# Optimization experiments

Hardware: AMD Instinct MI355X
Metric: run time of the kernel (lower is better)

## Reference

```python
import jax, jax.numpy as jnp
import numpy as np

B, T, D, H, W = 4096, 101, 64, 64, 32

# Tsit5 Butcher tableau (Tsitouras 2011), as used by diffrax.Tsit5
A21 = 0.161
A31, A32 = -0.008480655492356989, 0.335480655492357
A41, A42, A43 = 2.8971530571054935, -6.359448489975075, 4.3622954328695815
A51, A52, A53, A54 = 5.325864828439257, -11.748883564062828, 7.4955393428898365, -0.09249506636175525
A61, A62, A63, A64, A65 = 5.86145544294642, -12.92096931784711, 8.159367898576159, -0.071584973281401, -0.028269050394068383
# 5th-order solution weights (b7 = 0)
B1, B2, B3, B4, B5, B6 = 0.09646076681806523, 0.01, 0.4798896504144996, 1.379008574103742, -3.290069515436081, 2.324710524099774


def _mlp(y, W1, b1, W2, b2, W3, b3):
    # eqx.nn.MLP(hidden, hidden, width=32, depth=2, tanh): two tanh hidden layers
    h = jnp.tanh(y @ W1.T + b1)
    h = jnp.tanh(h @ W2.T + b2)
    return h @ W3.T + b3


def _tsit5_step(z, dt, p):
    f = lambda y: _mlp(y, *p)  # autonomous vector field (ignores t)
    k1 = f(z)
    k2 = f(z + dt * (A21 * k1))
    k3 = f(z + dt * (A31 * k1 + A32 * k2))
    k4 = f(z + dt * (A41 * k1 + A42 * k2 + A43 * k3))
    k5 = f(z + dt * (A51 * k1 + A52 * k2 + A53 * k3 + A54 * k4))
    k6 = f(z + dt * (A61 * k1 + A62 * k2 + A63 * k3 + A64 * k4 + A65 * k5))
    return z + dt * (B1 * k1 + B2 * k2 + B3 * k3 + B4 * k4 + B5 * k5 + B6 * k6)


def setup_inputs() -> dict:
    key = jax.random.key(0)
    ks = jax.random.split(key, 9)
    s = lambda fan_in: 1.0 / np.sqrt(fan_in)
    return {
        "ts": jnp.arange(T, dtype=jnp.float32) * 0.1,  # grid aligned with dt0=0.1
        "y0_batch": jax.random.normal(ks[0], (B, D), dtype=jnp.float32),
        "enc_W": jax.random.normal(ks[1], (H, D), dtype=jnp.float32) * s(D),
        "enc_b": jax.random.normal(ks[2], (H,), dtype=jnp.float32) * s(D),
        "W1": jax.random.normal(ks[3], (W, H), dtype=jnp.float32) * s(H),
        "b1": jnp.zeros((W,), dtype=jnp.float32),
        "W2": jax.random.normal(ks[4], (W, W), dtype=jnp.float32) * s(W),
        "b2": jnp.zeros((W,), dtype=jnp.float32),
        "W3": jax.random.normal(ks[5], (H, W), dtype=jnp.float32) * s(W),
        "b3": jnp.zeros((H,), dtype=jnp.float32),
        "dec_W": jax.random.normal(ks[6], (D, H), dtype=jnp.float32) * s(H),
        "dec_b": jax.random.normal(ks[7], (D,), dtype=jnp.float32) * s(H),
    }


def reference(ts, y0_batch, enc_W, enc_b, W1, b1, W2, b2, W3, b3, dec_W, dec_b):
    z0 = y0_batch @ enc_W.T + enc_b  # [B, H]
    n_steps = ts.shape[0] - 1
    dt = (ts[-1] - ts[0]) / n_steps  # == 0.1, matches dt0 with ConstantStepSize
    p = (W1, b1, W2, b2, W3, b3)

    def step(z, _):
        z1 = _tsit5_step(z, dt, p)
        return z1, z1

    _, zs_rest = jax.lax.scan(step, z0, None, length=n_steps)  # [T-1, B, H]
    zs = jnp.concatenate([z0[None], zs_rest], axis=0)  # [T, B, H]
    zs = jnp.swapaxes(zs, 0, 1)  # [B, T, H]
    ys = zs @ dec_W.T + dec_b  # [B, T, D]
    return ys, zs
```

## Files before the change

### kernel.cpp

```cpp
#include <hip/hip_runtime.h>


typedef __attribute__((ext_vector_type(8))) _Float16 half8;
typedef __attribute__((ext_vector_type(4))) float f32x4;

static constexpr int TN = 101;
static constexpr int BN = 4096;

#define MFMA(a, b, c) __builtin_amdgcn_mfma_f32_16x16x32_f16((a), (b), (c), 0, 0, 0)

__device__ __forceinline__ float tanh_pre(float x) {
  float e = __builtin_amdgcn_exp2f(x);
  float r = __builtin_amdgcn_rcpf(e + 1.0f);
  return __builtin_fmaf(-2.0f, r, 1.0f);
}

__device__ __forceinline__ void split8(const float* v, half8& hi, half8& lo) {
#pragma unroll
  for (int j = 0; j < 8; ++j) {
    _Float16 h = (_Float16)v[j];
    hi[j] = h;
    lo[j] = (_Float16)(v[j] - (float)h);
  }
}

__device__ __forceinline__ void load_wfrag(const float* __restrict__ W, int C, int row, int q,
                                           int kt, float scale, half8& hi, half8& lo) {
  const float* p = W + row * C + kt * 32 + 4 * q;
  float v[8] __attribute__((aligned(16)));
  *(f32x4*)(v) = *(const f32x4*)(p);
  *(f32x4*)(v + 4) = *(const f32x4*)(p + 16);
#pragma unroll
  for (int j = 0; j < 8; ++j) v[j] *= scale;
  split8(v, hi, lo);
}

__global__ __launch_bounds__(64, 1) void node_kernel(
    const float* __restrict__ ts, const float* __restrict__ y0,
    const float* __restrict__ encW, const float* __restrict__ encb,
    const float* __restrict__ W1, const float* __restrict__ b1,
    const float* __restrict__ W2, const float* __restrict__ b2,
    const float* __restrict__ W3, const float* __restrict__ b3,
    const float* __restrict__ decW, const float* __restrict__ decb,
    float* __restrict__ out) {
  const int l = threadIdx.x;
  const int lm = l & 15;
  const int q = l >> 4;
  const int eg = blockIdx.x * 16 + lm;

  const float TS = 2.8853900817779268f;

  const float dt = (ts[TN - 1] - ts[0]) / (float)(TN - 1);
  const float c21 = dt * 0.161f;
  const float c31 = dt * -0.008480655492356989f, c32 = dt * 0.335480655492357f;
  const float c41 = dt * 2.8971530571054935f, c42 = dt * -6.359448489975075f,
              c43 = dt * 4.3622954328695815f;
  const float c51 = dt * 5.325864828439257f, c52 = dt * -11.748883564062828f,
              c53 = dt * 7.4955393428898365f, c54 = dt * -0.09249506636175525f;
  const float c61 = dt * 5.86145544294642f, c62 = dt * -12.92096931784711f,
              c63 = dt * 8.159367898576159f, c64 = dt * -0.071584973281401f,
              c65 = dt * -0.028269050394068383f;
  const float d1 = dt * 0.09646076681806523f, d2 = dt * 0.01f, d3 = dt * 0.4798896504144996f,
              d4 = dt * 1.379008574103742f, d5 = dt * -3.290069515436081f,
              d6 = dt * 2.324710524099774f;
  const float sg3 = dt * 0.327f, sg4 = dt * 0.9f, sg5 = dt * 0.9800255409045097f,
              sg6 = dt * 1.0f;

  half8 w2h[2], w2l[2], w3h[4], w3l[4];
#pragma unroll
  for (int mt = 0; mt < 2; ++mt) load_wfrag(W2, 32, 16 * mt + lm, q, 0, TS, w2h[mt], w2l[mt]);
#pragma unroll
  for (int mt = 0; mt < 4; ++mt) load_wfrag(W3, 32, 16 * mt + lm, q, 0, 1.0f, w3h[mt], w3l[mt]);

  f32x4 b2f[2], db3f[4];
#pragma unroll
  for (int mt = 0; mt < 2; ++mt) {
    f32x4 t2 = *(const f32x4*)(b2 + 16 * mt + 4 * q);
#pragma unroll
    for (int r = 0; r < 4; ++r) t2[r] *= TS;
    b2f[mt] = t2;
  }
#pragma unroll
  for (int mt = 0; mt < 4; ++mt) {
    f32x4 t3 = *(const f32x4*)(b3 + 16 * mt + 4 * q);
#pragma unroll
    for (int r = 0; r < 4; ++r) t3[r] *= dt;
    db3f[mt] = t3;
  }

  half8 dech[4][2];
  f32x4 decbf[4];
#pragma unroll
  for (int mt = 0; mt < 4; ++mt) {
#pragma unroll
    for (int kt = 0; kt < 2; ++kt) {
      const float* p = decW + (16 * mt + lm) * 64 + kt * 32 + 4 * q;
      float v[8] __attribute__((aligned(16)));
      *(f32x4*)(v) = *(const f32x4*)(p);
      *(f32x4*)(v + 4) = *(const f32x4*)(p + 16);
      half8 h;
#pragma unroll
      for (int j = 0; j < 8; ++j) h[j] = (_Float16)v[j];
      dech[mt][kt] = h;
    }
    decbf[mt] = *(const f32x4*)(decb + 16 * mt + 4 * q);
  }

  half8 Mh[2], Ml[2];
  {
    float Mv0[8] = {0, 0, 0, 0, 0, 0, 0, 0};
    float Mv1[8] = {0, 0, 0, 0, 0, 0, 0, 0};
    const float* w1a = W1 + (size_t)lm * 64;
    const float* w1b = W1 + (size_t)(16 + lm) * 64;
    for (int k = 0; k < 64; ++k) {
      float a = w1a[k], b = w1b[k];
      const float* w3r = W3 + (size_t)k * 32 + 4 * q;
#pragma unroll
      for (int jj = 0; jj < 2; ++jj) {
#pragma unroll
        for (int r = 0; r < 4; ++r) {
          float w3v = w3r[16 * jj + r];
          Mv0[4 * jj + r] = __builtin_fmaf(a, w3v, Mv0[4 * jj + r]);
          Mv1[4 * jj + r] = __builtin_fmaf(b, w3v, Mv1[4 * jj + r]);
        }
      }
    }
#pragma unroll
    for (int j = 0; j < 8; ++j) {
      Mv0[j] *= TS;
      Mv1[j] *= TS;
    }
    split8(Mv0, Mh[0], Ml[0]);
    split8(Mv1, Mh[1], Ml[1]);
  }

  float c0[8] = {0, 0, 0, 0, 0, 0, 0, 0};
  {
    for (int k = 0; k < 64; ++k) {
      float bk = b3[k];
#pragma unroll
      for (int mt = 0; mt < 2; ++mt)
#pragma unroll
        for (int r = 0; r < 4; ++r)
          c0[4 * mt + r] =
              __builtin_fmaf(W1[(size_t)(16 * mt + 4 * q + r) * 64 + k], bk, c0[4 * mt + r]);
    }
#pragma unroll
    for (int j = 0; j < 8; ++j) c0[j] *= TS;
  }

  f32x4 zf[4];
  {
    const float* yp = y0 + (size_t)eg * 64;
    float v[16] __attribute__((aligned(16)));
    *(f32x4*)(v) = *(const f32x4*)(yp + 8 * q);
    *(f32x4*)(v + 4) = *(const f32x4*)(yp + 8 * q + 4);
    *(f32x4*)(v + 8) = *(const f32x4*)(yp + 32 + 8 * q);
    *(f32x4*)(v + 12) = *(const f32x4*)(yp + 32 + 8 * q + 4);
    half8 xh[2], xl[2];
    split8(v, xh[0], xl[0]);
    split8(v + 8, xh[1], xl[1]);
#pragma unroll
    for (int mt = 0; mt < 4; ++mt) {
      const float* p0 = encW + (16 * mt + lm) * 64 + 8 * q;
      float w[8] __attribute__((aligned(16)));
      half8 eh, el;
      f32x4 a = *(const f32x4*)(encb + 16 * mt + 4 * q);
      *(f32x4*)(w) = *(const f32x4*)(p0);
      *(f32x4*)(w + 4) = *(const f32x4*)(p0 + 4);
      split8(w, eh, el);
      a = MFMA(eh, xh[0], a);
      a = MFMA(el, xh[0], a);
      a = MFMA(eh, xl[0], a);
      *(f32x4*)(w) = *(const f32x4*)(p0 + 32);
      *(f32x4*)(w + 4) = *(const f32x4*)(p0 + 36);
      split8(w, eh, el);
      a = MFMA(eh, xh[1], a);
      a = MFMA(el, xh[1], a);
      a = MFMA(eh, xl[1], a);
      zf[mt] = a;
    }
  }

  float u[8];
  {
    half8 t1h[2][2], t1l[2][2];
    f32x4 tb1[2];
#pragma unroll
    for (int mt = 0; mt < 2; ++mt) {
#pragma unroll
      for (int kt = 0; kt < 2; ++kt)
        load_wfrag(W1, 64, 16 * mt + lm, q, kt, TS, t1h[mt][kt], t1l[mt][kt]);
      f32x4 t1 = *(const f32x4*)(b1 + 16 * mt + 4 * q);
#pragma unroll
      for (int r = 0; r < 4; ++r) t1[r] *= TS;
      tb1[mt] = t1;
    }
    float zv[16];
#pragma unroll
    for (int mt = 0; mt < 4; ++mt)
#pragma unroll
      for (int r = 0; r < 4; ++r) zv[4 * mt + r] = zf[mt][r];
    half8 yh[2], yl[2];
    split8(zv, yh[0], yl[0]);
    split8(zv + 8, yh[1], yl[1]);
#pragma unroll
    for (int mt = 0; mt < 2; ++mt) {
      f32x4 a = tb1[mt];
      a = MFMA(t1h[mt][0], yh[0], a);
      a = MFMA(t1l[mt][0], yh[0], a);
      a = MFMA(t1h[mt][0], yl[0], a);
      a = MFMA(t1h[mt][1], yh[1], a);
      a = MFMA(t1l[mt][1], yh[1], a);
      a = MFMA(t1h[mt][1], yl[1], a);
#pragma unroll
      for (int r = 0; r < 4; ++r) u[4 * mt + r] = a[r];
    }
  }

  auto store_z = [&](int s) {
    float* zb = out + (size_t)BN * TN * 64 + ((size_t)eg * TN + s) * 64;
#pragma unroll
    for (int mt = 0; mt < 4; ++mt) *(f32x4*)(zb + 16 * mt + 4 * q) = zf[mt];
  };
  auto dec_store = [&](int s) {
    half8 xh[2];
#pragma unroll
    for (int j = 0; j < 4; ++j) {
      xh[0][j] = (_Float16)zf[0][j];
      xh[0][4 + j] = (_Float16)zf[1][j];
      xh[1][j] = (_Float16)zf[2][j];
      xh[1][4 + j] = (_Float16)zf[3][j];
    }
    float* yb = out + ((size_t)eg * TN + s) * 64;
#pragma unroll
    for (int mt = 0; mt < 4; ++mt) {
      f32x4 a = decbf[mt];
      a = MFMA(dech[mt][0], xh[0], a);
      a = MFMA(dech[mt][1], xh[1], a);
      *(f32x4*)(yb + 16 * mt + 4 * q) = a;
    }
  };

  auto layerchain = [&](const float (&pin)[8], float (&h2o)[8], float (&mo)[8]) {
    float h1[8];
#pragma unroll
    for (int j = 0; j < 8; ++j) h1[j] = tanh_pre(pin[j]);
    half8 hh, hl;
    split8(h1, hh, hl);
    float qv[8];
#pragma unroll
    for (int mt = 0; mt < 2; ++mt) {
      f32x4 a = b2f[mt];
      a = MFMA(w2h[mt], hh, a);
      a = MFMA(w2l[mt], hh, a);
      a = MFMA(w2h[mt], hl, a);
#pragma unroll
      for (int r = 0; r < 4; ++r) qv[4 * mt + r] = a[r];
    }
#pragma unroll
    for (int j = 0; j < 8; ++j) h2o[j] = tanh_pre(qv[j]);
    half8 th, tl;
    split8(h2o, th, tl);
#pragma unroll
    for (int mt = 0; mt < 2; ++mt) {
      f32x4 a = {0.0f, 0.0f, 0.0f, 0.0f};
      a = MFMA(Mh[mt], th, a);
      a = MFMA(Ml[mt], th, a);
      a = MFMA(Mh[mt], tl, a);
#pragma unroll
      for (int r = 0; r < 4; ++r) mo[4 * mt + r] = a[r];
    }
  };

  float H[8];

  auto stages = [&]() {
    float U[8], P3[8], P4[8], P5[8], P6[8], p[8], h2[8], m[8];
#pragma unroll
    for (int j = 0; j < 8; ++j) {
      U[j] = __builtin_fmaf(dt, c0[j], u[j]);
      P3[j] = __builtin_fmaf(sg3, c0[j], u[j]);
      P4[j] = __builtin_fmaf(sg4, c0[j], u[j]);
      P5[j] = __builtin_fmaf(sg5, c0[j], u[j]);
      P6[j] = __builtin_fmaf(sg6, c0[j], u[j]);
    }
    layerchain(u, h2, m);
#pragma unroll
    for (int j = 0; j < 8; ++j) {
      H[j] = d1 * h2[j];
      U[j] = __builtin_fmaf(d1, m[j], U[j]);
      P3[j] = __builtin_fmaf(c31, m[j], P3[j]);
      P4[j] = __builtin_fmaf(c41, m[j], P4[j]);
      P5[j] = __builtin_fmaf(c51, m[j], P5[j]);
      P6[j] = __builtin_fmaf(c61, m[j], P6[j]);
      p[j] = __builtin_fmaf(c21, c0[j] + m[j], u[j]);
    }
    layerchain(p, h2, m);
#pragma unroll
    for (int j = 0; j < 8; ++j) {
      H[j] = __builtin_fmaf(d2, h2[j], H[j]);
      U[j] = __builtin_fmaf(d2, m[j], U[j]);
      P4[j] = __builtin_fmaf(c42, m[j], P4[j]);
      P5[j] = __builtin_fmaf(c52, m[j], P5[j]);
      P6[j] = __builtin_fmaf(c62, m[j], P6[j]);
      p[j] = __builtin_fmaf(c32, m[j], P3[j]);
    }
    layerchain(p, h2, m);
#pragma unroll
    for (int j = 0; j < 8; ++j) {
      H[j] = __builtin_fmaf(d3, h2[j], H[j]);
      U[j] = __builtin_fmaf(d3, m[j], U[j]);
      P5[j] = __builtin_fmaf(c53, m[j], P5[j]);
      P6[j] = __builtin_fmaf(c63, m[j], P6[j]);
      p[j] = __builtin_fmaf(c43, m[j], P4[j]);
    }
    layerchain(p, h2, m);
#pragma unroll
    for (int j = 0; j < 8; ++j) {
      H[j] = __builtin_fmaf(d4, h2[j], H[j]);
      U[j] = __builtin_fmaf(d4, m[j], U[j]);
      P6[j] = __builtin_fmaf(c64, m[j], P6[j]);
      p[j] = __builtin_fmaf(c54, m[j], P5[j]);
    }
    layerchain(p, h2, m);
#pragma unroll
    for (int j = 0; j < 8; ++j) {
      H[j] = __builtin_fmaf(d5, h2[j], H[j]);
      U[j] = __builtin_fmaf(d5, m[j], U[j]);
      p[j] = __builtin_fmaf(c65, m[j], P6[j]);
    }
    layerchain(p, h2, m);
#pragma unroll
    for (int j = 0; j < 8; ++j) {
      H[j] = __builtin_fmaf(d6, h2[j], H[j]);
      u[j] = __builtin_fmaf(d6, m[j], U[j]);
    }
  };

  auto zblock = [&](int s) {
    half8 Hh, Hl;
    split8(H, Hh, Hl);
#pragma unroll
    for (int mt = 0; mt < 4; ++mt) {
      f32x4 a = zf[mt];
      a = MFMA(w3h[mt], Hh, a);
      a = MFMA(w3l[mt], Hh, a);
      a = MFMA(w3h[mt], Hl, a);
      zf[mt] = a + db3f[mt];
    }
    store_z(s);
    dec_store(s);
  };

  store_z(0);
  dec_store(0);

  stages();
#pragma nounroll
  for (int s = 2; s < TN; ++s) {
    zblock(s - 1);
    stages();
  }
  zblock(TN - 1);
}

extern "C" void kernel_launch(void* const* d_in, const int* in_sizes, int n_in,
                              void* d_out, int out_size, void* d_ws, size_t ws_size,
                              hipStream_t stream) {
  const float* ts = (const float*)d_in[0];
  const float* y0 = (const float*)d_in[1];
  const float* encW = (const float*)d_in[2];
  const float* encb = (const float*)d_in[3];
  const float* W1 = (const float*)d_in[4];
  const float* b1 = (const float*)d_in[5];
  const float* W2 = (const float*)d_in[6];
  const float* b2 = (const float*)d_in[7];
  const float* W3 = (const float*)d_in[8];
  const float* b3 = (const float*)d_in[9];
  const float* decW = (const float*)d_in[10];
  const float* decb = (const float*)d_in[11];
  node_kernel<<<BN / 16, 64, 0, stream>>>(ts, y0, encW, encb, W1, b1, W2, b2, W3, b3, decW,
                                          decb, (float*)d_out);
}
```

Measured before the change: 469.5 us.

## Interleave two 16-row batch tiles per wavefront for instruction-level parallelism

Each 64-thread block now integrates 32 batch rows as two independent 16-row chains. Their MFMA and tanh operations are interleaved through all Tsit5 stages, the z update, the stores and the decoder, so one chain's work can hide the other's dependency latency. The grid halves to BN/32 blocks. With one wave per block, this roughly halves the number of active compute units and raises register pressure, trading device-wide parallelism for per-wave ILP.

```diff
diff --git a/kernel.cpp b/kernel.cpp
--- a/kernel.cpp
+++ b/kernel.cpp
@@ -46,7 +46,7 @@
   const int l = threadIdx.x;
   const int lm = l & 15;
   const int q = l >> 4;
-  const int eg = blockIdx.x * 16 + lm;
+  const int eg0 = blockIdx.x * 32 + lm;
 
   const float TS = 2.8853900817779268f;
 
@@ -149,9 +149,10 @@
     for (int j = 0; j < 8; ++j) c0[j] *= TS;
   }
 
-  f32x4 zf[4];
-  {
-    const float* yp = y0 + (size_t)eg * 64;
+  f32x4 zf[2][4];
+#pragma unroll
+  for (int c = 0; c < 2; ++c) {
+    const float* yp = y0 + (size_t)(eg0 + 16 * c) * 64;
     float v[16] __attribute__((aligned(16)));
     *(f32x4*)(v) = *(const f32x4*)(yp + 8 * q);
     *(f32x4*)(v + 4) = *(const f32x4*)(yp + 8 * q + 4);
@@ -178,11 +179,11 @@
       a = MFMA(eh, xh[1], a);
       a = MFMA(el, xh[1], a);
       a = MFMA(eh, xl[1], a);
-      zf[mt] = a;
-    }
-  }
-
-  float u[8];
+      zf[c][mt] = a;
+    }
+  }
+
+  float u[2][8];
   {
     half8 t1h[2][2], t1l[2][2];
     f32x4 tb1[2];
@@ -196,158 +197,204 @@
       for (int r = 0; r < 4; ++r) t1[r] *= TS;
       tb1[mt] = t1;
     }
-    float zv[16];
-#pragma unroll
-    for (int mt = 0; mt < 4; ++mt)
-#pragma unroll
-      for (int r = 0; r < 4; ++r) zv[4 * mt + r] = zf[mt][r];
-    half8 yh[2], yl[2];
-    split8(zv, yh[0], yl[0]);
-    split8(zv + 8, yh[1], yl[1]);
-#pragma unroll
-    for (int mt = 0; mt < 2; ++mt) {
-      f32x4 a = tb1[mt];
-      a = MFMA(t1h[mt][0], yh[0], a);
-      a = MFMA(t1l[mt][0], yh[0], a);
-      a = MFMA(t1h[mt][0], yl[0], a);
-      a = MFMA(t1h[mt][1], yh[1], a);
-      a = MFMA(t1l[mt][1], yh[1], a);
-      a = MFMA(t1h[mt][1], yl[1], a);
-#pragma unroll
-      for (int r = 0; r < 4; ++r) u[4 * mt + r] = a[r];
+#pragma unroll
+    for (int c = 0; c < 2; ++c) {
+      float zv[16];
+#pragma unroll
+      for (int mt = 0; mt < 4; ++mt)
+#pragma unroll
+        for (int r = 0; r < 4; ++r) zv[4 * mt + r] = zf[c][mt][r];
+      half8 yh[2], yl[2];
+      split8(zv, yh[0], yl[0]);
+      split8(zv + 8, yh[1], yl[1]);
+#pragma unroll
+      for (int mt = 0; mt < 2; ++mt) {
+        f32x4 a = tb1[mt];
+        a = MFMA(t1h[mt][0], yh[0], a);
+        a = MFMA(t1l[mt][0], yh[0], a);
+        a = MFMA(t1h[mt][0], yl[0], a);
+        a = MFMA(t1h[mt][1], yh[1], a);
+        a = MFMA(t1l[mt][1], yh[1], a);
+        a = MFMA(t1h[mt][1], yl[1], a);
+#pragma unroll
+        for (int r = 0; r < 4; ++r) u[c][4 * mt + r] = a[r];
+      }
     }
   }
 
   auto store_z = [&](int s) {
-    float* zb = out + (size_t)BN * TN * 64 + ((size_t)eg * TN + s) * 64;
-#pragma unroll
-    for (int mt = 0; mt < 4; ++mt) *(f32x4*)(zb + 16 * mt + 4 * q) = zf[mt];
+#pragma unroll
+    for (int c = 0; c < 2; ++c) {
+      float* zb = out + (size_t)BN * TN * 64 + ((size_t)(eg0 + 16 * c) * TN + s) * 64;
+#pragma unroll
+      for (int mt = 0; mt < 4; ++mt) *(f32x4*)(zb + 16 * mt + 4 * q) = zf[c][mt];
+    }
   };
   auto dec_store = [&](int s) {
-    half8 xh[2];
-#pragma unroll
-    for (int j = 0; j < 4; ++j) {
-      xh[0][j] = (_Float16)zf[0][j];
-      xh[0][4 + j] = (_Float16)zf[1][j];
-      xh[1][j] = (_Float16)zf[2][j];
-      xh[1][4 + j] = (_Float16)zf[3][j];
-    }
-    float* yb = out + ((size_t)eg * TN + s) * 64;
+#pragma unroll
+    for (int c = 0; c < 2; ++c) {
+      half8 xh[2];
+#pragma unroll
+      for (int j = 0; j < 4; ++j) {
+        xh[0][j] = (_Float16)zf[c][0][j];
+        xh[0][4 + j] = (_Float16)zf[c][1][j];
+        xh[1][j] = (_Float16)zf[c][2][j];
+        xh[1][4 + j] = (_Float16)zf[c][3][j];
+      }
+      float* yb = out + ((size_t)(eg0 + 16 * c) * TN + s) * 64;
+#pragma unroll
+      for (int mt = 0; mt < 4; ++mt) {
+        f32x4 a = decbf[mt];
+        a = MFMA(dech[mt][0], xh[0], a);
+        a = MFMA(dech[mt][1], xh[1], a);
+        *(f32x4*)(yb + 16 * mt + 4 * q) = a;
+      }
+    }
+  };
+
+  auto layerchain2 = [&](const float (&pin)[2][8], float (&h2o)[2][8], float (&mo)[2][8]) {
+    float h1[2][8];
+#pragma unroll
+    for (int c = 0; c < 2; ++c)
+#pragma unroll
+      for (int j = 0; j < 8; ++j) h1[c][j] = tanh_pre(pin[c][j]);
+    half8 hh[2], hl[2];
+    split8(h1[0], hh[0], hl[0]);
+    split8(h1[1], hh[1], hl[1]);
+    float qv[2][8];
+#pragma unroll
+    for (int mt = 0; mt < 2; ++mt) {
+      f32x4 a0 = b2f[mt], a1 = b2f[mt];
+      a0 = MFMA(w2h[mt], hh[0], a0);
+      a1 = MFMA(w2h[mt], hh[1], a1);
+      a0 = MFMA(w2l[mt], hh[0], a0);
+      a1 = MFMA(w2l[mt], hh[1], a1);
+      a0 = MFMA(w2h[mt], hl[0], a0);
+      a1 = MFMA(w2h[mt], hl[1], a1);
+#pragma unroll
+      for (int r = 0; r < 4; ++r) {
+        qv[0][4 * mt + r] = a0[r];
+        qv[1][4 * mt + r] = a1[r];
+      }
+    }
+#pragma unroll
+    for (int c = 0; c < 2; ++c)
+#pragma unroll
+      for (int j = 0; j < 8; ++j) h2o[c][j] = tanh_pre(qv[c][j]);
+    half8 th[2], tl[2];
+    split8(h2o[0], th[0], tl[0]);
+    split8(h2o[1], th[1], tl[1]);
+#pragma unroll
+    for (int mt = 0; mt < 2; ++mt) {
+      f32x4 a0 = {0.0f, 0.0f, 0.0f, 0.0f}, a1 = {0.0f, 0.0f, 0.0f, 0.0f};
+      a0 = MFMA(Mh[mt], th[0], a0);
+      a1 = MFMA(Mh[mt], th[1], a1);
+      a0 = MFMA(Ml[mt], th[0], a0);
+      a1 = MFMA(Ml[mt], th[1], a1);
+      a0 = MFMA(Mh[mt], tl[0], a0);
+      a1 = MFMA(Mh[mt], tl[1], a1);
+#pragma unroll
+      for (int r = 0; r < 4; ++r) {
+        mo[0][4 * mt + r] = a0[r];
+        mo[1][4 * mt + r] = a1[r];
+      }
+    }
+  };
+
+  float H[2][8];
+
+  auto stages = [&]() {
+    float U[2][8], P3[2][8], P4[2][8], P5[2][8], P6[2][8], p[2][8], h2[2][8], m[2][8];
+#pragma unroll
+    for (int c = 0; c < 2; ++c)
+#pragma unroll
+      for (int j = 0; j < 8; ++j) {
+        U[c][j] = __builtin_fmaf(dt, c0[j], u[c][j]);
+        P3[c][j] = __builtin_fmaf(sg3, c0[j], u[c][j]);
+        P4[c][j] = __builtin_fmaf(sg4, c0[j], u[c][j]);
+        P5[c][j] = __builtin_fmaf(sg5, c0[j], u[c][j]);
+        P6[c][j] = __builtin_fmaf(sg6, c0[j], u[c][j]);
+      }
+    layerchain2(u, h2, m);
+#pragma unroll
+    for (int c = 0; c < 2; ++c)
+#pragma unroll
+      for (int j = 0; j < 8; ++j) {
+        H[c][j] = d1 * h2[c][j];
+        U[c][j] = __builtin_fmaf(d1, m[c][j], U[c][j]);
+        P3[c][j] = __builtin_fmaf(c31, m[c][j], P3[c][j]);
+        P4[c][j] = __builtin_fmaf(c41, m[c][j], P4[c][j]);
+        P5[c][j] = __builtin_fmaf(c51, m[c][j], P5[c][j]);
+        P6[c][j] = __builtin_fmaf(c61, m[c][j], P6[c][j]);
+        p[c][j] = __builtin_fmaf(c21, c0[j] + m[c][j], u[c][j]);
+      }
+    layerchain2(p, h2, m);
+#pragma unroll
+    for (int c = 0; c < 2; ++c)
+#pragma unroll
+      for (int j = 0; j < 8; ++j) {
+        H[c][j] = __builtin_fmaf(d2, h2[c][j], H[c][j]);
+        U[c][j] = __builtin_fmaf(d2, m[c][j], U[c][j]);
+        P4[c][j] = __builtin_fmaf(c42, m[c][j], P4[c][j]);
+        P5[c][j] = __builtin_fmaf(c52, m[c][j], P5[c][j]);
+        P6[c][j] = __builtin_fmaf(c62, m[c][j], P6[c][j]);
+        p[c][j] = __builtin_fmaf(c32, m[c][j], P3[c][j]);
+      }
+    layerchain2(p, h2, m);
+#pragma unroll
+    for (int c = 0; c < 2; ++c)
+#pragma unroll
+      for (int j = 0; j < 8; ++j) {
+        H[c][j] = __builtin_fmaf(d3, h2[c][j], H[c][j]);
+        U[c][j] = __builtin_fmaf(d3, m[c][j], U[c][j]);
+        P5[c][j] = __builtin_fmaf(c53, m[c][j], P5[c][j]);
+        P6[c][j] = __builtin_fmaf(c63, m[c][j], P6[c][j]);
+        p[c][j] = __builtin_fmaf(c43, m[c][j], P4[c][j]);
+      }
+    layerchain2(p, h2, m);
+#pragma unroll
+    for (int c = 0; c < 2; ++c)
+#pragma unroll
+      for (int j = 0; j < 8; ++j) {
+        H[c][j] = __builtin_fmaf(d4, h2[c][j], H[c][j]);
+        U[c][j] = __builtin_fmaf(d4, m[c][j], U[c][j]);
+        P6[c][j] = __builtin_fmaf(c64, m[c][j], P6[c][j]);
+        p[c][j] = __builtin_fmaf(c54, m[c][j], P5[c][j]);
+      }
+    layerchain2(p, h2, m);
+#pragma unroll
+    for (int c = 0; c < 2; ++c)
+#pragma unroll
+      for (int j = 0; j < 8; ++j) {
+        H[c][j] = __builtin_fmaf(d5, h2[c][j], H[c][j]);
+        U[c][j] = __builtin_fmaf(d5, m[c][j], U[c][j]);
+        p[c][j] = __builtin_fmaf(c65, m[c][j], P6[c][j]);
+      }
+    layerchain2(p, h2, m);
+#pragma unroll
+    for (int c = 0; c < 2; ++c)
+#pragma unroll
+      for (int j = 0; j < 8; ++j) {
+        H[c][j] = __builtin_fmaf(d6, h2[c][j], H[c][j]);
+        u[c][j] = __builtin_fmaf(d6, m[c][j], U[c][j]);
+      }
+  };
+
+  auto zblock = [&](int s) {
+    half8 Hh[2], Hl[2];
+    split8(H[0], Hh[0], Hl[0]);
+    split8(H[1], Hh[1], Hl[1]);
 #pragma unroll
     for (int mt = 0; mt < 4; ++mt) {
-      f32x4 a = decbf[mt];
-      a = MFMA(dech[mt][0], xh[0], a);
-      a = MFMA(dech[mt][1], xh[1], a);
-      *(f32x4*)(yb + 16 * mt + 4 * q) = a;
-    }
-  };
-
-  auto layerchain = [&](const float (&pin)[8], float (&h2o)[8], float (&mo)[8]) {
-    float h1[8];
-#pragma unroll
-    for (int j = 0; j < 8; ++j) h1[j] = tanh_pre(pin[j]);
-    half8 hh, hl;
-    split8(h1, hh, hl);
-    float qv[8];
-#pragma unroll
-    for (int mt = 0; mt < 2; ++mt) {
-      f32x4 a = b2f[mt];
-      a = MFMA(w2h[mt], hh, a);
-      a = MFMA(w2l[mt], hh, a);
-      a = MFMA(w2h[mt], hl, a);
-#pragma unroll
-      for (int r = 0; r < 4; ++r) qv[4 * mt + r] = a[r];
-    }
-#pragma unroll
-    for (int j = 0; j < 8; ++j) h2o[j] = tanh_pre(qv[j]);
-    half8 th, tl;
-    split8(h2o, th, tl);
-#pragma unroll
-    for (int mt = 0; mt < 2; ++mt) {
-      f32x4 a = {0.0f, 0.0f, 0.0f, 0.0f};
-      a = MFMA(Mh[mt], th, a);
-      a = MFMA(Ml[mt], th, a);
-      a = MFMA(Mh[mt], tl, a);
-#pragma unroll
-      for (int r = 0; r < 4; ++r) mo[4 * mt + r] = a[r];
-    }
-  };
-
-  float H[8];
-
-  auto stages = [&]() {
-    float U[8], P3[8], P4[8], P5[8], P6[8], p[8], h2[8], m[8];
-#pragma unroll
-    for (int j = 0; j < 8; ++j) {
-      U[j] = __builtin_fmaf(dt, c0[j], u[j]);
-      P3[j] = __builtin_fmaf(sg3, c0[j], u[j]);
-      P4[j] = __builtin_fmaf(sg4, c0[j], u[j]);
-      P5[j] = __builtin_fmaf(sg5, c0[j], u[j]);
-      P6[j] = __builtin_fmaf(sg6, c0[j], u[j]);
-    }
-    layerchain(u, h2, m);
-#pragma unroll
-    for (int j = 0; j < 8; ++j) {
-      H[j] = d1 * h2[j];
-      U[j] = __builtin_fmaf(d1, m[j], U[j]);
-      P3[j] = __builtin_fmaf(c31, m[j], P3[j]);
-      P4[j] = __builtin_fmaf(c41, m[j], P4[j]);
-      P5[j] = __builtin_fmaf(c51, m[j], P5[j]);
-      P6[j] = __builtin_fmaf(c61, m[j], P6[j]);
-      p[j] = __builtin_fmaf(c21, c0[j] + m[j], u[j]);
-    }
-    layerchain(p, h2, m);
-#pragma unroll
-    for (int j = 0; j < 8; ++j) {
-      H[j] = __builtin_fmaf(d2, h2[j], H[j]);
-      U[j] = __builtin_fmaf(d2, m[j], U[j]);
-      P4[j] = __builtin_fmaf(c42, m[j], P4[j]);
-      P5[j] = __builtin_fmaf(c52, m[j], P5[j]);
-      P6[j] = __builtin_fmaf(c62, m[j], P6[j]);
-      p[j] = __builtin_fmaf(c32, m[j], P3[j]);
-    }
-    layerchain(p, h2, m);
-#pragma unroll
-    for (int j = 0; j < 8; ++j) {
-      H[j] = __builtin_fmaf(d3, h2[j], H[j]);
-      U[j] = __builtin_fmaf(d3, m[j], U[j]);
-      P5[j] = __builtin_fmaf(c53, m[j], P5[j]);
-      P6[j] = __builtin_fmaf(c63, m[j], P6[j]);
-      p[j] = __builtin_fmaf(c43, m[j], P4[j]);
-    }
-    layerchain(p, h2, m);
-#pragma unroll
-    for (int j = 0; j < 8; ++j) {
-      H[j] = __builtin_fmaf(d4, h2[j], H[j]);
-      U[j] = __builtin_fmaf(d4, m[j], U[j]);
-      P6[j] = __builtin_fmaf(c64, m[j], P6[j]);
-      p[j] = __builtin_fmaf(c54, m[j], P5[j]);
-    }
-    layerchain(p, h2, m);
-#pragma unroll
-    for (int j = 0; j < 8; ++j) {
-      H[j] = __builtin_fmaf(d5, h2[j], H[j]);
-      U[j] = __builtin_fmaf(d5, m[j], U[j]);
-      p[j] = __builtin_fmaf(c65, m[j], P6[j]);
-    }
-    layerchain(p, h2, m);
-#pragma unroll
-    for (int j = 0; j < 8; ++j) {
-      H[j] = __builtin_fmaf(d6, h2[j], H[j]);
-      u[j] = __builtin_fmaf(d6, m[j], U[j]);
-    }
-  };
-
-  auto zblock = [&](int s) {
-    half8 Hh, Hl;
-    split8(H, Hh, Hl);
-#pragma unroll
-    for (int mt = 0; mt < 4; ++mt) {
-      f32x4 a = zf[mt];
-      a = MFMA(w3h[mt], Hh, a);
-      a = MFMA(w3l[mt], Hh, a);
-      a = MFMA(w3h[mt], Hl, a);
-      zf[mt] = a + db3f[mt];
+      f32x4 a0 = zf[0][mt], a1 = zf[1][mt];
+      a0 = MFMA(w3h[mt], Hh[0], a0);
+      a1 = MFMA(w3h[mt], Hh[1], a1);
+      a0 = MFMA(w3l[mt], Hh[0], a0);
+      a1 = MFMA(w3l[mt], Hh[1], a1);
+      a0 = MFMA(w3h[mt], Hl[0], a0);
+      a1 = MFMA(w3h[mt], Hl[1], a1);
+      zf[0][mt] = a0 + db3f[mt];
+      zf[1][mt] = a1 + db3f[mt];
     }
     store_z(s);
     dec_store(s);
@@ -380,6 +427,6 @@
   const float* b3 = (const float*)d_in[9];
   const float* decW = (const float*)d_in[10];
   const float* decb = (const float*)d_in[11];
-  node_kernel<<<BN / 16, 64, 0, stream>>>(ts, y0, encW, encb, W1, b1, W2, b2, W3, b3, decW,
+  node_kernel<<<BN / 32, 64, 0, stream>>>(ts, y0, encW, encb, W1, b1, W2, b2, W3, b3, decW,
                                           decb, (float*)d_out);
 }
```

New measurement: 775.2 us. 65.1% more time.

## Split layer MFMAs into K=16 halves and interleave independent work between tanh halves

Applied to the files above, without the earlier changes.

Each MLP layer now runs as two K=16 MFMA halves, so the first half's matrix work can begin as soon as four tanh values are ready. Independent RK stage accumulations, the z update MFMAs, and the z/decoder stores from the previous step are injected between the tanh halves through callbacks. The aim is to hide MFMA and transcendental latency in a single-wave latency-bound chain. The cost is twice as many MFMA instructions, each smaller, plus more live registers. The z pre-subtraction and zero-initialised H let the first iteration reuse the fused pipeline.

```diff
diff --git a/kernel.cpp b/kernel.cpp
--- a/kernel.cpp
+++ b/kernel.cpp
@@ -2,12 +2,14 @@
 
 
 typedef __attribute__((ext_vector_type(8))) _Float16 half8;
+typedef __attribute__((ext_vector_type(4))) _Float16 half4;
 typedef __attribute__((ext_vector_type(4))) float f32x4;
 
 static constexpr int TN = 101;
 static constexpr int BN = 4096;
 
 #define MFMA(a, b, c) __builtin_amdgcn_mfma_f32_16x16x32_f16((a), (b), (c), 0, 0, 0)
+#define MFMA16(a, b, c) __builtin_amdgcn_mfma_f32_16x16x16f16((a), (b), (c), 0, 0, 0)
 
 __device__ __forceinline__ float tanh_pre(float x) {
   float e = __builtin_amdgcn_exp2f(x);
@@ -23,6 +25,18 @@
     lo[j] = (_Float16)(v[j] - (float)h);
   }
 }
+
+__device__ __forceinline__ void split4(const float* v, half4& hi, half4& lo) {
+#pragma unroll
+  for (int j = 0; j < 4; ++j) {
+    _Float16 h = (_Float16)v[j];
+    hi[j] = h;
+    lo[j] = (_Float16)(v[j] - (float)h);
+  }
+}
+
+__device__ __forceinline__ half4 lo4(half8 v) { return __builtin_shufflevector(v, v, 0, 1, 2, 3); }
+__device__ __forceinline__ half4 hi4(half8 v) { return __builtin_shufflevector(v, v, 4, 5, 6, 7); }
 
 __device__ __forceinline__ void load_wfrag(const float* __restrict__ W, int C, int row, int q,
                                            int kt, float scale, half8& hi, half8& lo) {
@@ -66,11 +80,20 @@
   const float sg3 = dt * 0.327f, sg4 = dt * 0.9f, sg5 = dt * 0.9800255409045097f,
               sg6 = dt * 1.0f;
 
-  half8 w2h[2], w2l[2], w3h[4], w3l[4];
-#pragma unroll
-  for (int mt = 0; mt < 2; ++mt) load_wfrag(W2, 32, 16 * mt + lm, q, 0, TS, w2h[mt], w2l[mt]);
+  half8 w2h8[2], w2l8[2], w3h[4], w3l[4];
+#pragma unroll
+  for (int mt = 0; mt < 2; ++mt) load_wfrag(W2, 32, 16 * mt + lm, q, 0, TS, w2h8[mt], w2l8[mt]);
 #pragma unroll
   for (int mt = 0; mt < 4; ++mt) load_wfrag(W3, 32, 16 * mt + lm, q, 0, 1.0f, w3h[mt], w3l[mt]);
+
+  half4 w2h4[2][2], w2l4[2][2];
+#pragma unroll
+  for (int mt = 0; mt < 2; ++mt) {
+    w2h4[mt][0] = lo4(w2h8[mt]);
+    w2h4[mt][1] = hi4(w2h8[mt]);
+    w2l4[mt][0] = lo4(w2l8[mt]);
+    w2l4[mt][1] = hi4(w2l8[mt]);
+  }
 
   f32x4 b2f[2], db3f[4];
 #pragma unroll
@@ -106,7 +129,7 @@
     decbf[mt] = *(const f32x4*)(decb + 16 * mt + 4 * q);
   }
 
-  half8 Mh[2], Ml[2];
+  half4 Mh4[2][2], Ml4[2][2];
   {
     float Mv0[8] = {0, 0, 0, 0, 0, 0, 0, 0};
     float Mv1[8] = {0, 0, 0, 0, 0, 0, 0, 0};
@@ -130,8 +153,17 @@
       Mv0[j] *= TS;
       Mv1[j] *= TS;
     }
-    split8(Mv0, Mh[0], Ml[0]);
-    split8(Mv1, Mh[1], Ml[1]);
+    half8 Mh8, Ml8;
+    split8(Mv0, Mh8, Ml8);
+    Mh4[0][0] = lo4(Mh8);
+    Mh4[0][1] = hi4(Mh8);
+    Ml4[0][0] = lo4(Ml8);
+    Ml4[0][1] = hi4(Ml8);
+    split8(Mv1, Mh8, Ml8);
+    Mh4[1][0] = lo4(Mh8);
+    Mh4[1][1] = hi4(Mh8);
+    Ml4[1][0] = lo4(Ml8);
+    Ml4[1][1] = hi4(Ml8);
   }
 
   float c0[8] = {0, 0, 0, 0, 0, 0, 0, 0};
@@ -242,103 +274,201 @@
     }
   };
 
-  auto layerchain = [&](const float (&pin)[8], float (&h2o)[8], float (&mo)[8]) {
-    float h1[8];
-#pragma unroll
-    for (int j = 0; j < 8; ++j) h1[j] = tanh_pre(pin[j]);
-    half8 hh, hl;
-    split8(h1, hh, hl);
+  auto LC = [&](const float (&pin)[8], float (&h2o)[8], float (&mo)[8], auto&& F0, auto&& F1,
+                auto&& F2, auto&& F3) {
+    float ha[4], hb[4];
+    half4 hah, hal, hbh, hbl;
+#pragma unroll
+    for (int j = 0; j < 4; ++j) ha[j] = tanh_pre(pin[j]);
+    F0();
+    split4(ha, hah, hal);
+#pragma unroll
+    for (int j = 0; j < 4; ++j) hb[j] = tanh_pre(pin[4 + j]);
+    F1();
+    split4(hb, hbh, hbl);
     float qv[8];
 #pragma unroll
     for (int mt = 0; mt < 2; ++mt) {
       f32x4 a = b2f[mt];
-      a = MFMA(w2h[mt], hh, a);
-      a = MFMA(w2l[mt], hh, a);
-      a = MFMA(w2h[mt], hl, a);
+      a = MFMA16(w2h4[mt][0], hah, a);
+      a = MFMA16(w2l4[mt][0], hah, a);
+      a = MFMA16(w2h4[mt][0], hal, a);
+      a = MFMA16(w2h4[mt][1], hbh, a);
+      a = MFMA16(w2l4[mt][1], hbh, a);
+      a = MFMA16(w2h4[mt][1], hbl, a);
 #pragma unroll
       for (int r = 0; r < 4; ++r) qv[4 * mt + r] = a[r];
     }
-#pragma unroll
-    for (int j = 0; j < 8; ++j) h2o[j] = tanh_pre(qv[j]);
-    half8 th, tl;
-    split8(h2o, th, tl);
+    half4 th0, tl0, th1, tl1;
+#pragma unroll
+    for (int j = 0; j < 4; ++j) h2o[j] = tanh_pre(qv[j]);
+    F2();
+    split4(h2o, th0, tl0);
+#pragma unroll
+    for (int j = 0; j < 4; ++j) h2o[4 + j] = tanh_pre(qv[4 + j]);
+    F3();
+    split4(h2o + 4, th1, tl1);
 #pragma unroll
     for (int mt = 0; mt < 2; ++mt) {
       f32x4 a = {0.0f, 0.0f, 0.0f, 0.0f};
-      a = MFMA(Mh[mt], th, a);
-      a = MFMA(Ml[mt], th, a);
-      a = MFMA(Mh[mt], tl, a);
+      a = MFMA16(Mh4[mt][0], th0, a);
+      a = MFMA16(Ml4[mt][0], th0, a);
+      a = MFMA16(Mh4[mt][0], tl0, a);
+      a = MFMA16(Mh4[mt][1], th1, a);
+      a = MFMA16(Ml4[mt][1], th1, a);
+      a = MFMA16(Mh4[mt][1], tl1, a);
 #pragma unroll
       for (int r = 0; r < 4; ++r) mo[4 * mt + r] = a[r];
     }
   };
 
   float H[8];
-
-  auto stages = [&]() {
-    float U[8], P3[8], P4[8], P5[8], P6[8], p[8], h2[8], m[8];
+#pragma unroll
+  for (int j = 0; j < 8; ++j) H[j] = 0.0f;
+#pragma unroll
+  for (int mt = 0; mt < 4; ++mt) zf[mt] = zf[mt] - db3f[mt];
+
+#pragma nounroll
+  for (int s = 1; s < TN; ++s) {
+    float U[8], P3[8], P4[8], P5[8], P6[8], pv[8], mA[8], mB[8], h2A[8], h2B[8];
+    half8 Hh, Hl;
+    LC(u, h2A, mA,
+       [&] {
+         split8(H, Hh, Hl);
+#pragma unroll
+         for (int j = 0; j < 8; ++j) {
+           U[j] = __builtin_fmaf(dt, c0[j], u[j]);
+           P3[j] = __builtin_fmaf(sg3, c0[j], u[j]);
+         }
+       },
+       [&] {
+#pragma unroll
+         for (int mt = 0; mt < 2; ++mt) {
+           f32x4 a = zf[mt];
+           a = MFMA(w3h[mt], Hh, a);
+           a = MFMA(w3l[mt], Hh, a);
+           a = MFMA(w3h[mt], Hl, a);
+           zf[mt] = a + db3f[mt];
+         }
+#pragma unroll
+         for (int j = 0; j < 8; ++j) {
+           P4[j] = __builtin_fmaf(sg4, c0[j], u[j]);
+           P5[j] = __builtin_fmaf(sg5, c0[j], u[j]);
+         }
+       },
+       [&] {
+#pragma unroll
+         for (int mt = 2; mt < 4; ++mt) {
+           f32x4 a = zf[mt];
+           a = MFMA(w3h[mt], Hh, a);
+           a = MFMA(w3l[mt], Hh, a);
+           a = MFMA(w3h[mt], Hl, a);
+           zf[mt] = a + db3f[mt];
+         }
+#pragma unroll
+         for (int j = 0; j < 8; ++j) P6[j] = __builtin_fmaf(sg6, c0[j], u[j]);
+         store_z(s - 1);
+       },
+       [&] { dec_store(s - 1); });
+#pragma unroll
+    for (int j = 0; j < 8; ++j) pv[j] = __builtin_fmaf(c21, c0[j] + mA[j], u[j]);
+    LC(pv, h2B, mB,
+       [&] {
+#pragma unroll
+         for (int j = 0; j < 8; ++j) {
+           H[j] = d1 * h2A[j];
+           U[j] = __builtin_fmaf(d1, mA[j], U[j]);
+         }
+       },
+       [&] {
+#pragma unroll
+         for (int j = 0; j < 8; ++j) {
+           P3[j] = __builtin_fmaf(c31, mA[j], P3[j]);
+           P4[j] = __builtin_fmaf(c41, mA[j], P4[j]);
+         }
+       },
+       [&] {
+#pragma unroll
+         for (int j = 0; j < 8; ++j) P5[j] = __builtin_fmaf(c51, mA[j], P5[j]);
+       },
+       [&] {
+#pragma unroll
+         for (int j = 0; j < 8; ++j) P6[j] = __builtin_fmaf(c61, mA[j], P6[j]);
+       });
+#pragma unroll
+    for (int j = 0; j < 8; ++j) pv[j] = __builtin_fmaf(c32, mB[j], P3[j]);
+    LC(pv, h2A, mA,
+       [&] {
+#pragma unroll
+         for (int j = 0; j < 8; ++j) {
+           H[j] = __builtin_fmaf(d2, h2B[j], H[j]);
+           U[j] = __builtin_fmaf(d2, mB[j], U[j]);
+         }
+       },
+       [&] {
+#pragma unroll
+         for (int j = 0; j < 8; ++j) {
+           P4[j] = __builtin_fmaf(c42, mB[j], P4[j]);
+           P5[j] = __builtin_fmaf(c52, mB[j], P5[j]);
+         }
+       },
+       [&] {
+#pragma unroll
+         for (int j = 0; j < 8; ++j) P6[j] = __builtin_fmaf(c62, mB[j], P6[j]);
+       },
+       [&] {});
+#pragma unroll
+    for (int j = 0; j < 8; ++j) pv[j] = __builtin_fmaf(c43, mA[j], P4[j]);
+    LC(pv, h2B, mB,
+       [&] {
+#pragma unroll
+         for (int j = 0; j < 8; ++j) {
+           H[j] = __builtin_fmaf(d3, h2A[j], H[j]);
+           U[j] = __builtin_fmaf(d3, mA[j], U[j]);
+         }
+       },
+       [&] {
+#pragma unroll
+         for (int j = 0; j < 8; ++j) {
+           P5[j] = __builtin_fmaf(c53, mA[j], P5[j]);
+           P6[j] = __builtin_fmaf(c63, mA[j], P6[j]);
+         }
+       },
+       [&] {}, [&] {});
+#pragma unroll
+    for (int j = 0; j < 8; ++j) pv[j] = __builtin_fmaf(c54, mB[j], P5[j]);
+    LC(pv, h2A, mA,
+       [&] {
+#pragma unroll
+         for (int j = 0; j < 8; ++j) {
+           H[j] = __builtin_fmaf(d4, h2B[j], H[j]);
+           U[j] = __builtin_fmaf(d4, mB[j], U[j]);
+         }
+       },
+       [&] {
+#pragma unroll
+         for (int j = 0; j < 8; ++j) P6[j] = __builtin_fmaf(c64, mB[j], P6[j]);
+       },
+       [&] {}, [&] {});
+#pragma unroll
+    for (int j = 0; j < 8; ++j) pv[j] = __builtin_fmaf(c65, mA[j], P6[j]);
+    LC(pv, h2B, mB,
+       [&] {
+#pragma unroll
+         for (int j = 0; j < 8; ++j) {
+           H[j] = __builtin_fmaf(d5, h2A[j], H[j]);
+           U[j] = __builtin_fmaf(d5, mA[j], U[j]);
+         }
+       },
+       [&] {}, [&] {}, [&] {});
 #pragma unroll
     for (int j = 0; j < 8; ++j) {
-      U[j] = __builtin_fmaf(dt, c0[j], u[j]);
-      P3[j] = __builtin_fmaf(sg3, c0[j], u[j]);
-      P4[j] = __builtin_fmaf(sg4, c0[j], u[j]);
-      P5[j] = __builtin_fmaf(sg5, c0[j], u[j]);
-      P6[j] = __builtin_fmaf(sg6, c0[j], u[j]);
-    }
-    layerchain(u, h2, m);
-#pragma unroll
-    for (int j = 0; j < 8; ++j) {
-      H[j] = d1 * h2[j];
-      U[j] = __builtin_fmaf(d1, m[j], U[j]);
-      P3[j] = __builtin_fmaf(c31, m[j], P3[j]);
-      P4[j] = __builtin_fmaf(c41, m[j], P4[j]);
-      P5[j] = __builtin_fmaf(c51, m[j], P5[j]);
-      P6[j] = __builtin_fmaf(c61, m[j], P6[j]);
-      p[j] = __builtin_fmaf(c21, c0[j] + m[j], u[j]);
-    }
-    layerchain(p, h2, m);
-#pragma unroll
-    for (int j = 0; j < 8; ++j) {
-      H[j] = __builtin_fmaf(d2, h2[j], H[j]);
-      U[j] = __builtin_fmaf(d2, m[j], U[j]);
-      P4[j] = __builtin_fmaf(c42, m[j], P4[j]);
-      P5[j] = __builtin_fmaf(c52, m[j], P5[j]);
-      P6[j] = __builtin_fmaf(c62, m[j], P6[j]);
-      p[j] = __builtin_fmaf(c32, m[j], P3[j]);
-    }
-    layerchain(p, h2, m);
-#pragma unroll
-    for (int j = 0; j < 8; ++j) {
-      H[j] = __builtin_fmaf(d3, h2[j], H[j]);
-      U[j] = __builtin_fmaf(d3, m[j], U[j]);
-      P5[j] = __builtin_fmaf(c53, m[j], P5[j]);
-      P6[j] = __builtin_fmaf(c63, m[j], P6[j]);
-      p[j] = __builtin_fmaf(c43, m[j], P4[j]);
-    }
-    layerchain(p, h2, m);
-#pragma unroll
-    for (int j = 0; j < 8; ++j) {
-      H[j] = __builtin_fmaf(d4, h2[j], H[j]);
-      U[j] = __builtin_fmaf(d4, m[j], U[j]);
-      P6[j] = __builtin_fmaf(c64, m[j], P6[j]);
-      p[j] = __builtin_fmaf(c54, m[j], P5[j]);
-    }
-    layerchain(p, h2, m);
-#pragma unroll
-    for (int j = 0; j < 8; ++j) {
-      H[j] = __builtin_fmaf(d5, h2[j], H[j]);
-      U[j] = __builtin_fmaf(d5, m[j], U[j]);
-      p[j] = __builtin_fmaf(c65, m[j], P6[j]);
-    }
-    layerchain(p, h2, m);
-#pragma unroll
-    for (int j = 0; j < 8; ++j) {
-      H[j] = __builtin_fmaf(d6, h2[j], H[j]);
-      u[j] = __builtin_fmaf(d6, m[j], U[j]);
-    }
-  };
-
-  auto zblock = [&](int s) {
+      H[j] = __builtin_fmaf(d6, h2B[j], H[j]);
+      u[j] = __builtin_fmaf(d6, mB[j], U[j]);
+    }
+  }
+
+  {
     half8 Hh, Hl;
     split8(H, Hh, Hl);
 #pragma unroll
@@ -349,20 +479,9 @@
       a = MFMA(w3h[mt], Hl, a);
       zf[mt] = a + db3f[mt];
     }
-    store_z(s);
-    dec_store(s);
-  };
-
-  store_z(0);
-  dec_store(0);
-
-  stages();
-#pragma nounroll
-  for (int s = 2; s < TN; ++s) {
-    zblock(s - 1);
-    stages();
-  }
-  zblock(TN - 1);
+    store_z(TN - 1);
+    dec_store(TN - 1);
+  }
 }
 
 extern "C" void kernel_launch(void* const* d_in, const int* in_sizes, int n_in,
```

After: 494.0 us. 1.05x slower.
